# Kernel tuning notes

Hardware: AMD Instinct MI355X
Metric: run time of the kernel (lower is better)

The kernel has to match this reference:

```python
import jax, jax.numpy as jnp
import numpy as np

EPS_BIAS = 1e-6  # bias_epsilon

def _l2n(x, axis):
    # F.normalize: x / clamp_min(||x||, 1e-12)
    return x / jnp.maximum(jnp.linalg.norm(x, axis=axis, keepdims=True), 1e-12)

def _se3_W(w):
    # convex completion: rows sum to 1
    return jnp.concatenate([w, 1.0 - w.sum(-1, keepdims=True)], axis=-1)

def _vlin(v, W):
    # channel-mixing linear over dim 1 of [B, C, 3, N]
    return jnp.einsum('oc,bcdn->bodn', W, v)

def _vec_sub(v, w, b, se3):
    # sub VecLinear with s_in=s_out=0: linear + tiny normalized bias
    W = _se3_W(w) if se3 else w
    out = _vlin(v, W)
    bias = (_l2n(b, -1) * EPS_BIAS).reshape(1, -1, 1, 1)
    return out + bias

def _cev_norm(x):
    # channel_equi_vec_normalize
    d = _l2n(x, 2)
    n = jnp.linalg.norm(x, axis=2, keepdims=True)
    return d * _l2n(n, 1)

def setup_inputs() -> dict:
    key = jax.random.key(0)
    B, v_in, v_out, s_in, s_out, N = 8, 128, 128, 64, 64, 4096
    ks = jax.random.split(key, 16)
    def w(k, shape, fan):
        return jax.random.normal(k, shape, jnp.float32) / np.float32(np.sqrt(fan))
    return {
        'v_input': jax.random.normal(ks[0], (B, v_in, 3, N), jnp.float32),
        's_input': jax.random.normal(ks[1], (B, s_in, N), jnp.float32),
        'weight':   w(ks[2], (v_out, v_in - 1), v_in) + 1.0 / v_in,
        'sv_w':     w(ks[3], (v_out, s_in), s_in),
        'sv_b':     w(ks[4], (v_out,), s_in),
        'cross_w':  w(ks[5], (v_out, v_in - 1), v_in) + 1.0 / v_in,
        'cross_b':  jax.random.normal(ks[6], (v_out,), jnp.float32),
        'crossfc_w': w(ks[7], (v_out, 2 * v_out - 1), 2 * v_out) + 1.0 / (2 * v_out),
        'crossfc_b': jax.random.normal(ks[8], (v_out,), jnp.float32),
        'vsdir_w':  w(ks[9], (v_in, v_in), v_in),
        'vsdir_b':  jax.random.normal(ks[10], (v_in,), jnp.float32),
        'vs_w':     w(ks[11], (s_out, v_in), v_in),
        'vs_b':     w(ks[12], (s_out,), v_in),
        'ss_w':     w(ks[13], (s_out, s_in), s_in),
        'ss_b':     w(ks[14], (s_out,), s_in),
    }

def reference(v_input, s_input, weight, sv_w, sv_b, cross_w, cross_b,
              crossfc_w, crossfc_b, vsdir_w, vsdir_b, vs_w, vs_b, ss_w, ss_b):
    # --- vector linear (sim3/se3: convex weights) ---
    v_o = _vlin(v_input, _se3_W(weight))                      # [B, v_out, 3, N]
    # --- scalar -> vector invariant scale (normalized over channels) ---
    scale = jnp.einsum('os,bsn->bon', sv_w, s_input) + sv_b[None, :, None]
    scale = _l2n(scale, 1)                                    # [B, v_out, N]
    m = v_o.mean(axis=1, keepdims=True)
    v_o = (v_o - m) * scale[:, :, None, :] + m
    # --- cross-product branch ---
    v_dual = _vec_sub(v_input, cross_w, cross_b, True)
    dual_o = v_dual.mean(axis=1, keepdims=True)
    out_o = v_o.mean(axis=1, keepdims=True)
    v_cross = jnp.cross(_cev_norm(v_dual - dual_o), v_o - out_o, axis=2) + v_o
    v_o = _vec_sub(jnp.concatenate([v_cross, v_o], axis=1), crossfc_w, crossfc_b, True)
    # --- vector -> scalar (invariant) ---
    v_sR = v_input - v_input.mean(axis=1, keepdims=True)
    dual_dir = _l2n(_vec_sub(v_sR, vsdir_w, vsdir_b, False), 2)  # so3 sub-module
    s_from_v = _l2n((v_sR * dual_dir).sum(axis=2), 1)         # [B, v_in, N]
    s_from_v = jnp.einsum('oc,bcn->bon', vs_w, s_from_v) + vs_b[None, :, None]
    s_from_s = jnp.einsum('os,bsn->bon', ss_w, s_input) + ss_b[None, :, None]
    return v_o, s_from_s + s_from_v
```

## Files before the change

### kernel.cpp

```cpp
#include <hip/hip_runtime.h>

#define VOUT_ELEMS 12582912

typedef __attribute__((ext_vector_type(8))) short bf16x8;
typedef __attribute__((ext_vector_type(4))) float f32x4;

__device__ __forceinline__ unsigned short f2b(float f) {
  unsigned x = __float_as_uint(f);
  x = (x + 0x7FFFu + ((x >> 16) & 1u)) >> 16;
  return (unsigned short)x;
}
__device__ __forceinline__ float b2f(unsigned short u) {
  return __uint_as_float(((unsigned)u) << 16);
}
__device__ __forceinline__ unsigned pk2(float a, float b) {
  unsigned r;
  asm("v_cvt_pk_bf16_f32 %0, %1, %2" : "=v"(r) : "v"(a), "v"(b));
  return r;
}


__global__ void kprep0(const float* __restrict__ weight, const float* __restrict__ cross_w,
                       const float* __restrict__ crossfc_w, const float* __restrict__ vsdir_w,
                       const float* __restrict__ cross_b, const float* __restrict__ crossfc_b,
                       const float* __restrict__ vsdir_b, float* __restrict__ wsf)
{
  const int tid = threadIdx.x;
  const int l = tid & 63;
  const int wg = blockIdx.x*4 + (tid>>6);
#pragma unroll
  for (int k = 0; k < 2; ++k) {
    int o = wg*2 + k;
    float a = weight[o*127+l]  + ((l<63) ? weight[o*127+64+l]  : 0.f);
    float b = cross_w[o*127+l] + ((l<63) ? cross_w[o*127+64+l] : 0.f);
    float f = crossfc_w[o*255+l] + crossfc_w[o*255+64+l] + crossfc_w[o*255+128+l]
            + ((l<63) ? crossfc_w[o*255+192+l] : 0.f);
    float v = vsdir_w[o*128+l] + vsdir_w[o*128+64+l];
#pragma unroll
    for (int m = 1; m < 64; m <<= 1) {
      a += __shfl_xor(a,m,64); b += __shfl_xor(b,m,64);
      f += __shfl_xor(f,m,64); v += __shfl_xor(v,m,64);
    }
    if (l == 0) {
      wsf[384+o] = a; wsf[512+o] = b; wsf[640+o] = f; wsf[768+o] = v*(1.f/128.f);
    }
  }
  if (blockIdx.x == 0 && tid < 192) {
    const float* bsrc = (tid < 64) ? cross_b : (tid < 128 ? crossfc_b : vsdir_b);
    float a = 0.f;
    for (int i = l; i < 128; i += 64) { float t = bsrc[i]; a += t*t; }
#pragma unroll
    for (int m = 1; m < 64; m <<= 1) a += __shfl_xor(a,m,64);
    float nb = fmaxf(sqrtf(a), 1e-12f);
    for (int i = l; i < 128; i += 64)
      wsf[(tid>>6)*128 + i] = bsrc[i] / nb * 1e-6f;
  }
}

__global__ void kprep1(const float* __restrict__ weight, const float* __restrict__ sv_w,
                       const float* __restrict__ cross_w, const float* __restrict__ crossfc_w,
                       const float* __restrict__ vsdir_w, const float* __restrict__ vs_w,
                       const float* __restrict__ ss_w,
                       unsigned short* __restrict__ wsb, const float* __restrict__ wsf)
{
  const int stride = 64*256;
  const int base = blockIdx.x*256 + threadIdx.x;
  const float* rs1 = wsf+384; const float* rs2 = wsf+512;
  const float* rsF = wsf+640; const float* vdm = wsf+768;
  for (int i = base; i < 16384; i += stride) {
    int j=i&7, lane=(i>>3)&63, ks=(i>>9)&3, mt=i>>11;
    int o=16*mt+(lane&15), cc=32*ks+8*(lane>>4)+j;
    wsb[i]       = f2b(cc<127 ? weight[o*127+cc]  : 1.f-rs1[o]);
    wsb[16384+i] = f2b(cc<127 ? cross_w[o*127+cc] : 1.f-rs2[o]);
    wsb[65536+i] = f2b(vsdir_w[o*128+cc] - vdm[o]);
  }
  for (int i = base; i < 32768; i += stride) {
    int j=i&7, lane=(i>>3)&63, ks=(i>>9)&7, mt=i>>12;
    int o=16*mt+(lane&15), cc=32*ks+8*(lane>>4)+j;
    wsb[32768+i] = f2b(cc<255 ? crossfc_w[o*255+cc] : 1.f-rsF[o]);
  }
  for (int i = base; i < 8192; i += stride) {
    int j=i&7, lane=(i>>3)&63, ks=(i>>9)&1, mt=i>>10;
    int o=16*mt+(lane&15), s=32*ks+8*(lane>>4)+j;
    wsb[81920+i] = f2b(sv_w[o*64+s]);
  }
  for (int i = base; i < 8192; i += stride) {
    int j=i&7, lane=(i>>3)&63, ks=(i>>9)&3, mt=i>>11;
    int o=16*mt+(lane&15), c=32*ks+8*(lane>>4)+j;
    wsb[90112+i] = f2b(vs_w[o*128+c]);
  }
  for (int i = base; i < 4096; i += stride) {
    int j=i&7, lane=(i>>3)&63, ks=(i>>9)&1, mt=i>>10;
    int o=16*mt+(lane&15), s=32*ks+8*(lane>>4)+j;
    wsb[98304+i] = f2b(ss_w[o*64+s]);
  }
}

__global__ __launch_bounds__(256, 4) void kmain(
    const float* __restrict__ v_in, const float* __restrict__ s_in,
    const float* __restrict__ sv_b, const float* __restrict__ vs_b,
    const float* __restrict__ ss_b,
    const unsigned short* __restrict__ wsb, const float* __restrict__ wsf,
    float* __restrict__ out_v, float* __restrict__ out_s)
{
  __shared__ __align__(16) unsigned char smem[31744];
  unsigned short* bfr = (unsigned short*)smem;
  float* gmx          = (float*)(smem + 12288);
  float (*gred)[16][4]  = (float(*)[16][4])(smem + 12480);
  unsigned short* sfr = (unsigned short*)(smem + 24576);
  unsigned short* vfr = (unsigned short*)(smem + 26624);
  float (*gred2)[16][4] = (float(*)[16][4])(smem + 30720);

  const int tid = threadIdx.x;
  const int w = tid >> 6, l = tid & 63, h = l >> 4, c15 = l & 15;
  const int n0 = blockIdx.x * 16;
  const size_t bb = blockIdx.y;
  const size_t vbase = bb*384*4096 + n0;
  const size_t sbase = bb*64*4096 + n0;

  for (int i = tid; i < 384; i += 256) {
    int q = i & 3, d = (i >> 2) % 3, cq = i / 12;
    const float* src = &v_in[vbase + (size_t)(4*cq*3 + d)*4096 + 4*q];
    float4 x0 = *(const float4*)(src);
    float4 x1 = *(const float4*)(src + 3*4096);
    float4 x2 = *(const float4*)(src + 6*4096);
    float4 x3 = *(const float4*)(src + 9*4096);
    int slot = (cq >> 3)*3 + d;
    int hh = (cq >> 1) & 3;
    int jp = 2*(cq & 1);
    unsigned* bp = (unsigned*)bfr + (slot*64 + 16*hh + 4*q)*4 + jp;
    float a0[4]={x0.x,x0.y,x0.z,x0.w}, a1[4]={x1.x,x1.y,x1.z,x1.w};
    float a2[4]={x2.x,x2.y,x2.z,x2.w}, a3[4]={x3.x,x3.y,x3.z,x3.w};
#pragma unroll
    for (int e=0;e<4;++e)
      *(uint2*)(bp + e*4) = make_uint2(pk2(a0[e],a1[e]), pk2(a2[e],a3[e]));
  }
  if (tid < 64) {
    int q = tid & 3, sq = tid >> 2;
    const float* src = &s_in[sbase + (size_t)(4*sq)*4096 + 4*q];
    float4 x0 = *(const float4*)(src);
    float4 x1 = *(const float4*)(src + 4096);
    float4 x2 = *(const float4*)(src + 2*4096);
    float4 x3 = *(const float4*)(src + 3*4096);
    int slot = sq >> 3;
    int hh = (sq >> 1) & 3;
    int jp = 2*(sq & 1);
    unsigned* bp = (unsigned*)sfr + (slot*64 + 16*hh + 4*q)*4 + jp;
    float a0[4]={x0.x,x0.y,x0.z,x0.w}, a1[4]={x1.x,x1.y,x1.z,x1.w};
    float a2[4]={x2.x,x2.y,x2.z,x2.w}, a3[4]={x3.x,x3.y,x3.z,x3.w};
#pragma unroll
    for (int e=0;e<4;++e)
      *(uint2*)(bp + e*4) = make_uint2(pk2(a0[e],a1[e]), pk2(a2[e],a3[e]));
  }
  __syncthreads();

  const bf16x8* bv  = (const bf16x8*)bfr;
  const bf16x8* sfv_p = (const bf16x8*)sfr;
  const bf16x8* vfv_p = (const bf16x8*)vfr;
  const bf16x8* wv  = (const bf16x8*)wsb;
  const int obA = 16*w + 4*h, obB = 16*(w+4) + 4*h;

  f32x4 avo[2][3], adu[2][3], adr[2][3], asc[2];
  {
    f32x4 b2A = *(const f32x4*)&wsf[obA],     b2B = *(const f32x4*)&wsf[obB];
    f32x4 bdA = *(const f32x4*)&wsf[256+obA], bdB = *(const f32x4*)&wsf[256+obB];
#pragma unroll
    for (int d=0;d<3;++d) {
      avo[0][d]=(f32x4){0.f,0.f,0.f,0.f}; avo[1][d]=(f32x4){0.f,0.f,0.f,0.f};
      adu[0][d]=b2A; adu[1][d]=b2B;
      adr[0][d]=bdA; adr[1][d]=bdB;
    }
    asc[0] = *(const f32x4*)&sv_b[obA];
    asc[1] = *(const f32x4*)&sv_b[obB];
  }
#pragma unroll
  for (int ks=0;ks<4;++ks) {
    bf16x8 bx[3];
#pragma unroll
    for (int d=0;d<3;++d) bx[d] = bv[(ks*3+d)*64 + l];
#pragma unroll
    for (int mt=0;mt<2;++mt) {
      int fa = (w + 4*mt)*4 + ks;
      bf16x8 a1 = wv[fa*64 + l];
      bf16x8 a2 = wv[2048 + fa*64 + l];
      bf16x8 a3 = wv[8192 + fa*64 + l];
#pragma unroll
      for (int d=0;d<3;++d) {
        avo[mt][d] = __builtin_amdgcn_mfma_f32_16x16x32_bf16(a1, bx[d], avo[mt][d], 0,0,0);
        adu[mt][d] = __builtin_amdgcn_mfma_f32_16x16x32_bf16(a2, bx[d], adu[mt][d], 0,0,0);
        adr[mt][d] = __builtin_amdgcn_mfma_f32_16x16x32_bf16(a3, bx[d], adr[mt][d], 0,0,0);
      }
    }
  }
#pragma unroll
  for (int ks=0;ks<2;++ks) {
    bf16x8 bs = sfv_p[ks*64 + l];
#pragma unroll
    for (int mt=0;mt<2;++mt) {
      bf16x8 a4 = wv[10240 + ((w+4*mt)*2+ks)*64 + l];
      asc[mt] = __builtin_amdgcn_mfma_f32_16x16x32_bf16(a4, bs, asc[mt], 0,0,0);
    }
  }
  if (w < 3) {
    bf16x8 aone;
#pragma unroll
    for (int j=0;j<8;++j) aone[j] = (short)0x3C00;
    f32x4 amx = (f32x4){0.f,0.f,0.f,0.f};
#pragma unroll
    for (int ks=0;ks<4;++ks)
      amx = __builtin_amdgcn_mfma_f32_16x16x32_bf16(aone, bv[(ks*3+w)*64+l], amx, 0,0,0);
    if (h==0) gmx[16*w + c15] = amx[0];
  }

  {
    float red[8];
#pragma unroll
    for (int d=0;d<3;++d) {
      red[d]   = avo[0][d][0]+avo[0][d][1]+avo[0][d][2]+avo[0][d][3]
               + avo[1][d][0]+avo[1][d][1]+avo[1][d][2]+avo[1][d][3];
      red[3+d] = adu[0][d][0]+adu[0][d][1]+adu[0][d][2]+adu[0][d][3]
               + adu[1][d][0]+adu[1][d][1]+adu[1][d][2]+adu[1][d][3];
    }
    float q2 = 0.f;
#pragma unroll
    for (int mt=0;mt<2;++mt)
#pragma unroll
      for (int d=0;d<3;++d)
#pragma unroll
        for (int r=0;r<4;++r) q2 += adu[mt][d][r]*adu[mt][d][r];
    red[6] = q2;
    red[7] = asc[0][0]*asc[0][0]+asc[0][1]*asc[0][1]+asc[0][2]*asc[0][2]+asc[0][3]*asc[0][3]
           + asc[1][0]*asc[1][0]+asc[1][1]*asc[1][1]+asc[1][2]*asc[1][2]+asc[1][3]*asc[1][3];
#pragma unroll
    for (int m=16;m<64;m<<=1)
#pragma unroll
      for (int i=0;i<8;++i) red[i] += __shfl_xor(red[i], m, 64);
    if (h==0)
#pragma unroll
      for (int i=0;i<8;++i) gred[i][c15][w] = red[i];
  }
  __syncthreads();

  float mvo[3], mdu[3], mxv[3], d2s, sinv;
#pragma unroll
  for (int d=0;d<3;++d) {
    f32x4 t = *(const f32x4*)gred[d][c15];
    f32x4 u = *(const f32x4*)gred[3+d][c15];
    mvo[d] = (t[0]+t[1]+t[2]+t[3]) * (1.f/128.f);
    mdu[d] = (u[0]+u[1]+u[2]+u[3]) * (1.f/128.f);
    mxv[d] = gmx[16*d + c15];
  }
  { f32x4 t = *(const f32x4*)gred[6][c15]; d2s = t[0]+t[1]+t[2]+t[3]; }
  { f32x4 t = *(const f32x4*)gred[7][c15];
    sinv = 1.f / fmaxf(sqrtf(t[0]+t[1]+t[2]+t[3]), 1e-12f); }

  float po[3] = {0.f,0.f,0.f};
#pragma unroll
  for (int mt=0;mt<2;++mt)
#pragma unroll
    for (int r=0;r<4;++r) {
      float sk = asc[mt][r] * sinv;
#pragma unroll
      for (int d=0;d<3;++d) {
        float t = (avo[mt][d][r]-mvo[d])*sk + mvo[d];
        avo[mt][d][r] = t;
        po[d] += t;
      }
    }

  float sfvv[2][4]; float pfn = 0.f;
#pragma unroll
  for (int mt=0;mt<2;++mt) {
    int c0 = 16*(w+4*mt) + 4*h;
    int ks = c0 >> 5, hh = (c0>>3)&3, ju = 2*(h&1);
    float xr[3][4];
#pragma unroll
    for (int d=0;d<3;++d) {
      uint2 u = *(const uint2*)((const unsigned*)bfr + ((ks*3+d)*64 + 16*hh + c15)*4 + ju);
      xr[d][0]=b2f((unsigned short)u.x);  xr[d][1]=b2f((unsigned short)(u.x>>16));
      xr[d][2]=b2f((unsigned short)u.y);  xr[d][3]=b2f((unsigned short)(u.y>>16));
    }
#pragma unroll
    for (int r=0;r<4;++r) {
      float dx=adr[mt][0][r], dy=adr[mt][1][r], dz=adr[mt][2][r];
      float rn = sqrtf(dx*dx+dy*dy+dz*dz);
      float inv = 1.f/fmaxf(rn,1e-12f);
      float vx = xr[0][r]-mxv[0], vy = xr[1][r]-mxv[1], vz = xr[2][r]-mxv[2];
      float dot = (vx*dx+vy*dy+vz*dz)*inv;
      sfvv[mt][r] = dot; pfn += dot*dot;
    }
  }

  {
    float red2[4] = {po[0], po[1], po[2], pfn};
#pragma unroll
    for (int m=16;m<64;m<<=1)
#pragma unroll
      for (int i=0;i<4;++i) red2[i] += __shfl_xor(red2[i], m, 64);
    if (h==0)
#pragma unroll
      for (int i=0;i<4;++i) gred2[i][c15][w] = red2[i];
  }
  __syncthreads();

  float moo[3], sfni;
#pragma unroll
  for (int d=0;d<3;++d) {
    f32x4 t = *(const f32x4*)gred2[d][c15];
    moo[d] = (t[0]+t[1]+t[2]+t[3]) * (1.f/128.f);
  }
  { f32x4 t = *(const f32x4*)gred2[3][c15];
    sfni = 1.f/fmaxf(sqrtf(t[0]+t[1]+t[2]+t[3]), 1e-12f); }

  float m2 = mdu[0]*mdu[0]+mdu[1]*mdu[1]+mdu[2]*mdu[2];
  float F  = sqrtf(fmaxf(d2s - 128.f*m2, 0.f));
  float Fi = 1.f/fmaxf(F, 1e-12f);
#pragma unroll
  for (int mt=0;mt<2;++mt) {
    int c0 = 16*(w+4*mt) + 4*h;
    int ks = c0 >> 5, hh = (c0>>3)&3, ju = 2*(h&1);
    *(uint2*)((unsigned*)vfr + (ks*64 + 16*hh + c15)*4 + ju) =
      make_uint2(pk2(sfvv[mt][0]*sfni, sfvv[mt][1]*sfni),
                 pk2(sfvv[mt][2]*sfni, sfvv[mt][3]*sfni));
    float cv[3][4];
#pragma unroll
    for (int r=0;r<4;++r) {
      float ax=adu[mt][0][r]-mdu[0], ay=adu[mt][1][r]-mdu[1], az=adu[mt][2][r]-mdu[2];
      float rn = sqrtf(ax*ax+ay*ay+az*az);
      float s1 = (rn*Fi)/fmaxf(rn,1e-12f);
      ax*=s1; ay*=s1; az*=s1;
      float bx=avo[mt][0][r]-moo[0], by=avo[mt][1][r]-moo[1], bz=avo[mt][2][r]-moo[2];
      cv[0][r]=ay*bz-az*by+avo[mt][0][r];
      cv[1][r]=az*bx-ax*bz+avo[mt][1][r];
      cv[2][r]=ax*by-ay*bx+avo[mt][2][r];
    }
#pragma unroll
    for (int d=0;d<3;++d) {
      *(uint2*)((unsigned*)bfr + ((ks*3+d)*64 + 16*hh + c15)*4 + ju) =
        make_uint2(pk2(cv[d][0],cv[d][1]), pk2(cv[d][2],cv[d][3]));
      *(uint2*)((unsigned*)bfr + (((4+ks)*3+d)*64 + 16*hh + c15)*4 + ju) =
        make_uint2(pk2(avo[mt][d][0],avo[mt][d][1]), pk2(avo[mt][d][2],avo[mt][d][3]));
    }
  }
  __syncthreads();

  f32x4 afc[2][3];
  {
    f32x4 bfA = *(const f32x4*)&wsf[128+obA], bfB = *(const f32x4*)&wsf[128+obB];
#pragma unroll
    for (int d=0;d<3;++d) { afc[0][d]=bfA; afc[1][d]=bfB; }
  }
#pragma unroll
  for (int ks=0;ks<8;++ks) {
    bf16x8 bx[3];
#pragma unroll
    for (int d=0;d<3;++d) bx[d] = bv[(ks*3+d)*64 + l];
#pragma unroll
    for (int mt=0;mt<2;++mt) {
      bf16x8 a5 = wv[4096 + ((w+4*mt)*8+ks)*64 + l];
#pragma unroll
      for (int d=0;d<3;++d)
        afc[mt][d] = __builtin_amdgcn_mfma_f32_16x16x32_bf16(a5, bx[d], afc[mt][d], 0,0,0);
    }
  }
  f32x4 as2;
  {
    f32x4 bv1 = *(const f32x4*)&vs_b[obA];
    f32x4 bv2 = *(const f32x4*)&ss_b[obA];
    as2 = (f32x4){bv1[0]+bv2[0], bv1[1]+bv2[1], bv1[2]+bv2[2], bv1[3]+bv2[3]};
  }
#pragma unroll
  for (int ks=0;ks<4;++ks) {
    bf16x8 a6 = wv[11264 + (w*4+ks)*64 + l];
    as2 = __builtin_amdgcn_mfma_f32_16x16x32_bf16(a6, vfv_p[ks*64+l], as2, 0,0,0);
  }
#pragma unroll
  for (int ks=0;ks<2;++ks) {
    bf16x8 a7 = wv[12288 + (w*2+ks)*64 + l];
    as2 = __builtin_amdgcn_mfma_f32_16x16x32_bf16(a7, sfv_p[ks*64+l], as2, 0,0,0);
  }

#pragma unroll
  for (int mt=0;mt<2;++mt) {
    int c0 = 16*(w+4*mt) + 4*h;
#pragma unroll
    for (int d=0;d<3;++d)
#pragma unroll
      for (int r=0;r<4;++r)
        out_v[vbase + (size_t)((c0+r)*3 + d)*4096 + c15] = afc[mt][d][r];
  }
#pragma unroll
  for (int r=0;r<4;++r)
    out_s[sbase + (size_t)(obA+r)*4096 + c15] = as2[r];
}

extern "C" void kernel_launch(void* const* d_in, const int* in_sizes, int n_in,
                              void* d_out, int out_size, void* d_ws, size_t ws_size,
                              hipStream_t stream) {
  (void)in_sizes; (void)n_in; (void)out_size; (void)ws_size;
  const float* v_in      = (const float*)d_in[0];
  const float* s_in      = (const float*)d_in[1];
  const float* weight    = (const float*)d_in[2];
  const float* sv_w      = (const float*)d_in[3];
  const float* sv_b      = (const float*)d_in[4];
  const float* cross_w   = (const float*)d_in[5];
  const float* cross_b   = (const float*)d_in[6];
  const float* crossfc_w = (const float*)d_in[7];
  const float* crossfc_b = (const float*)d_in[8];
  const float* vsdir_w   = (const float*)d_in[9];
  const float* vsdir_b   = (const float*)d_in[10];
  const float* vs_w      = (const float*)d_in[11];
  const float* vs_b      = (const float*)d_in[12];
  const float* ss_w      = (const float*)d_in[13];
  const float* ss_b      = (const float*)d_in[14];

  unsigned short* wsb = (unsigned short*)d_ws;
  float* wsf = (float*)((char*)d_ws + 204800);

  kprep0<<<16, 256, 0, stream>>>(weight, cross_w, crossfc_w, vsdir_w,
                                 cross_b, crossfc_b, vsdir_b, wsf);
  kprep1<<<64, 256, 0, stream>>>(weight, sv_w, cross_w, crossfc_w, vsdir_w,
                                 vs_w, ss_w, wsb, wsf);
  dim3 grid(4096/16, 8);
  kmain<<<grid, 256, 0, stream>>>(v_in, s_in, sv_b, vs_b, ss_b, wsb, wsf,
                                  (float*)d_out, (float*)d_out + VOUT_ELEMS);
}
```

Before: 64.31 us.

## Fold second block reduction into first via algebraic mean and deferred normalization

Removes the second __syncthreads and its reduction round. The mean of the scaled v_o is now computed algebraically from extra first-pass sums (sum of avo*asc and sum of asc). The input-channel mean is computed by reduction instead of the ones-MFMA. The s_from_v normalization is deferred past the vs GEMM, since it is linear, and applied as a per-column scale at output, using the pfn reduction written to shared memory before the existing FC barrier. This costs more shuffle reductions (15 values instead of 8), more shared memory, and a bf16 rounding difference because unnormalized values are packed.

```diff
diff --git a/kernel.cpp b/kernel.cpp
--- a/kernel.cpp
+++ b/kernel.cpp
@@ -103,13 +103,12 @@
     const unsigned short* __restrict__ wsb, const float* __restrict__ wsf,
     float* __restrict__ out_v, float* __restrict__ out_s)
 {
-  __shared__ __align__(16) unsigned char smem[31744];
+  __shared__ __align__(16) unsigned char smem[34816];
   unsigned short* bfr = (unsigned short*)smem;
-  float* gmx          = (float*)(smem + 12288);
-  float (*gred)[16][4]  = (float(*)[16][4])(smem + 12480);
   unsigned short* sfr = (unsigned short*)(smem + 24576);
   unsigned short* vfr = (unsigned short*)(smem + 26624);
-  float (*gred2)[16][4] = (float(*)[16][4])(smem + 30720);
+  float (*gred)[16][4]  = (float(*)[16][4])(smem + 30720);
+  float (*gred2)[4]     = (float(*)[4])(smem + 34560);
 
   const int tid = threadIdx.x;
   const int w = tid >> 6, l = tid & 63, h = l >> 4, c15 = l & 15;
@@ -201,25 +200,34 @@
       asc[mt] = __builtin_amdgcn_mfma_f32_16x16x32_bf16(a4, bs, asc[mt], 0,0,0);
     }
   }
-  if (w < 3) {
-    bf16x8 aone;
-#pragma unroll
-    for (int j=0;j<8;++j) aone[j] = (short)0x3C00;
-    f32x4 amx = (f32x4){0.f,0.f,0.f,0.f};
-#pragma unroll
-    for (int ks=0;ks<4;++ks)
-      amx = __builtin_amdgcn_mfma_f32_16x16x32_bf16(aone, bv[(ks*3+w)*64+l], amx, 0,0,0);
-    if (h==0) gmx[16*w + c15] = amx[0];
+
+  float xr[2][3][4];
+#pragma unroll
+  for (int mt=0;mt<2;++mt) {
+    int c0 = 16*(w+4*mt) + 4*h;
+    int ksq = c0 >> 5, hh = (c0>>3)&3, ju = 2*(h&1);
+#pragma unroll
+    for (int d=0;d<3;++d) {
+      uint2 u = *(const uint2*)((const unsigned*)bfr + ((ksq*3+d)*64 + 16*hh + c15)*4 + ju);
+      xr[mt][d][0]=b2f((unsigned short)u.x);  xr[mt][d][1]=b2f((unsigned short)(u.x>>16));
+      xr[mt][d][2]=b2f((unsigned short)u.y);  xr[mt][d][3]=b2f((unsigned short)(u.y>>16));
+    }
   }
 
   {
-    float red[8];
+    float red[15];
 #pragma unroll
     for (int d=0;d<3;++d) {
       red[d]   = avo[0][d][0]+avo[0][d][1]+avo[0][d][2]+avo[0][d][3]
                + avo[1][d][0]+avo[1][d][1]+avo[1][d][2]+avo[1][d][3];
       red[3+d] = adu[0][d][0]+adu[0][d][1]+adu[0][d][2]+adu[0][d][3]
                + adu[1][d][0]+adu[1][d][1]+adu[1][d][2]+adu[1][d][3];
+      red[8+d] = avo[0][d][0]*asc[0][0]+avo[0][d][1]*asc[0][1]
+               + avo[0][d][2]*asc[0][2]+avo[0][d][3]*asc[0][3]
+               + avo[1][d][0]*asc[1][0]+avo[1][d][1]*asc[1][1]
+               + avo[1][d][2]*asc[1][2]+avo[1][d][3]*asc[1][3];
+      red[12+d] = xr[0][d][0]+xr[0][d][1]+xr[0][d][2]+xr[0][d][3]
+                + xr[1][d][0]+xr[1][d][1]+xr[1][d][2]+xr[1][d][3];
     }
     float q2 = 0.f;
 #pragma unroll
@@ -231,86 +239,60 @@
     red[6] = q2;
     red[7] = asc[0][0]*asc[0][0]+asc[0][1]*asc[0][1]+asc[0][2]*asc[0][2]+asc[0][3]*asc[0][3]
            + asc[1][0]*asc[1][0]+asc[1][1]*asc[1][1]+asc[1][2]*asc[1][2]+asc[1][3]*asc[1][3];
+    red[11]= asc[0][0]+asc[0][1]+asc[0][2]+asc[0][3]
+           + asc[1][0]+asc[1][1]+asc[1][2]+asc[1][3];
 #pragma unroll
     for (int m=16;m<64;m<<=1)
 #pragma unroll
-      for (int i=0;i<8;++i) red[i] += __shfl_xor(red[i], m, 64);
+      for (int i=0;i<15;++i) red[i] += __shfl_xor(red[i], m, 64);
     if (h==0)
 #pragma unroll
-      for (int i=0;i<8;++i) gred[i][c15][w] = red[i];
+      for (int i=0;i<15;++i) gred[i][c15][w] = red[i];
   }
   __syncthreads();
 
-  float mvo[3], mdu[3], mxv[3], d2s, sinv;
+  float mvo[3], mdu[3], mxv[3], moo[3], d2s, sinv, Sa;
+  { f32x4 t = *(const f32x4*)gred[7][c15];
+    sinv = 1.f / fmaxf(sqrtf(t[0]+t[1]+t[2]+t[3]), 1e-12f); }
+  { f32x4 t = *(const f32x4*)gred[11][c15]; Sa = t[0]+t[1]+t[2]+t[3]; }
+  { f32x4 t = *(const f32x4*)gred[6][c15];  d2s = t[0]+t[1]+t[2]+t[3]; }
 #pragma unroll
   for (int d=0;d<3;++d) {
     f32x4 t = *(const f32x4*)gred[d][c15];
     f32x4 u = *(const f32x4*)gred[3+d][c15];
+    f32x4 v = *(const f32x4*)gred[8+d][c15];
+    f32x4 x = *(const f32x4*)gred[12+d][c15];
     mvo[d] = (t[0]+t[1]+t[2]+t[3]) * (1.f/128.f);
     mdu[d] = (u[0]+u[1]+u[2]+u[3]) * (1.f/128.f);
-    mxv[d] = gmx[16*d + c15];
-  }
-  { f32x4 t = *(const f32x4*)gred[6][c15]; d2s = t[0]+t[1]+t[2]+t[3]; }
-  { f32x4 t = *(const f32x4*)gred[7][c15];
-    sinv = 1.f / fmaxf(sqrtf(t[0]+t[1]+t[2]+t[3]), 1e-12f); }
-
-  float po[3] = {0.f,0.f,0.f};
+    float Svs = v[0]+v[1]+v[2]+v[3];
+    moo[d] = mvo[d] + sinv*(Svs - mvo[d]*Sa)*(1.f/128.f);
+    mxv[d] = (x[0]+x[1]+x[2]+x[3]) * (1.f/128.f);
+  }
+
 #pragma unroll
   for (int mt=0;mt<2;++mt)
 #pragma unroll
     for (int r=0;r<4;++r) {
       float sk = asc[mt][r] * sinv;
 #pragma unroll
-      for (int d=0;d<3;++d) {
-        float t = (avo[mt][d][r]-mvo[d])*sk + mvo[d];
-        avo[mt][d][r] = t;
-        po[d] += t;
-      }
+      for (int d=0;d<3;++d)
+        avo[mt][d][r] = (avo[mt][d][r]-mvo[d])*sk + mvo[d];
     }
 
   float sfvv[2][4]; float pfn = 0.f;
 #pragma unroll
-  for (int mt=0;mt<2;++mt) {
-    int c0 = 16*(w+4*mt) + 4*h;
-    int ks = c0 >> 5, hh = (c0>>3)&3, ju = 2*(h&1);
-    float xr[3][4];
-#pragma unroll
-    for (int d=0;d<3;++d) {
-      uint2 u = *(const uint2*)((const unsigned*)bfr + ((ks*3+d)*64 + 16*hh + c15)*4 + ju);
-      xr[d][0]=b2f((unsigned short)u.x);  xr[d][1]=b2f((unsigned short)(u.x>>16));
-      xr[d][2]=b2f((unsigned short)u.y);  xr[d][3]=b2f((unsigned short)(u.y>>16));
-    }
+  for (int mt=0;mt<2;++mt)
 #pragma unroll
     for (int r=0;r<4;++r) {
       float dx=adr[mt][0][r], dy=adr[mt][1][r], dz=adr[mt][2][r];
       float rn = sqrtf(dx*dx+dy*dy+dz*dz);
       float inv = 1.f/fmaxf(rn,1e-12f);
-      float vx = xr[0][r]-mxv[0], vy = xr[1][r]-mxv[1], vz = xr[2][r]-mxv[2];
+      float vx = xr[mt][0][r]-mxv[0], vy = xr[mt][1][r]-mxv[1], vz = xr[mt][2][r]-mxv[2];
       float dot = (vx*dx+vy*dy+vz*dz)*inv;
       sfvv[mt][r] = dot; pfn += dot*dot;
     }
-  }
-
-  {
-    float red2[4] = {po[0], po[1], po[2], pfn};
-#pragma unroll
-    for (int m=16;m<64;m<<=1)
-#pragma unroll
-      for (int i=0;i<4;++i) red2[i] += __shfl_xor(red2[i], m, 64);
-    if (h==0)
-#pragma unroll
-      for (int i=0;i<4;++i) gred2[i][c15][w] = red2[i];
-  }
-  __syncthreads();
-
-  float moo[3], sfni;
-#pragma unroll
-  for (int d=0;d<3;++d) {
-    f32x4 t = *(const f32x4*)gred2[d][c15];
-    moo[d] = (t[0]+t[1]+t[2]+t[3]) * (1.f/128.f);
-  }
-  { f32x4 t = *(const f32x4*)gred2[3][c15];
-    sfni = 1.f/fmaxf(sqrtf(t[0]+t[1]+t[2]+t[3]), 1e-12f); }
+  pfn += __shfl_xor(pfn,16,64); pfn += __shfl_xor(pfn,32,64);
+  if (h==0) gred2[c15][w] = pfn;
 
   float m2 = mdu[0]*mdu[0]+mdu[1]*mdu[1]+mdu[2]*mdu[2];
   float F  = sqrtf(fmaxf(d2s - 128.f*m2, 0.f));
@@ -318,10 +300,9 @@
 #pragma unroll
   for (int mt=0;mt<2;++mt) {
     int c0 = 16*(w+4*mt) + 4*h;
-    int ks = c0 >> 5, hh = (c0>>3)&3, ju = 2*(h&1);
-    *(uint2*)((unsigned*)vfr + (ks*64 + 16*hh + c15)*4 + ju) =
-      make_uint2(pk2(sfvv[mt][0]*sfni, sfvv[mt][1]*sfni),
-                 pk2(sfvv[mt][2]*sfni, sfvv[mt][3]*sfni));
+    int ksq = c0 >> 5, hh = (c0>>3)&3, ju = 2*(h&1);
+    *(uint2*)((unsigned*)vfr + (ksq*64 + 16*hh + c15)*4 + ju) =
+      make_uint2(pk2(sfvv[mt][0], sfvv[mt][1]), pk2(sfvv[mt][2], sfvv[mt][3]));
     float cv[3][4];
 #pragma unroll
     for (int r=0;r<4;++r) {
@@ -336,9 +317,9 @@
     }
 #pragma unroll
     for (int d=0;d<3;++d) {
-      *(uint2*)((unsigned*)bfr + ((ks*3+d)*64 + 16*hh + c15)*4 + ju) =
+      *(uint2*)((unsigned*)bfr + ((ksq*3+d)*64 + 16*hh + c15)*4 + ju) =
         make_uint2(pk2(cv[d][0],cv[d][1]), pk2(cv[d][2],cv[d][3]));
-      *(uint2*)((unsigned*)bfr + (((4+ks)*3+d)*64 + 16*hh + c15)*4 + ju) =
+      *(uint2*)((unsigned*)bfr + (((4+ksq)*3+d)*64 + 16*hh + c15)*4 + ju) =
         make_uint2(pk2(avo[mt][d][0],avo[mt][d][1]), pk2(avo[mt][d][2],avo[mt][d][3]));
     }
   }
@@ -363,22 +344,26 @@
         afc[mt][d] = __builtin_amdgcn_mfma_f32_16x16x32_bf16(a5, bx[d], afc[mt][d], 0,0,0);
     }
   }
-  f32x4 as2;
+  f32x4 as_v = (f32x4){0.f,0.f,0.f,0.f};
+#pragma unroll
+  for (int ks=0;ks<4;++ks) {
+    bf16x8 a6 = wv[11264 + (w*4+ks)*64 + l];
+    as_v = __builtin_amdgcn_mfma_f32_16x16x32_bf16(a6, vfv_p[ks*64+l], as_v, 0,0,0);
+  }
+  f32x4 as_s;
   {
     f32x4 bv1 = *(const f32x4*)&vs_b[obA];
     f32x4 bv2 = *(const f32x4*)&ss_b[obA];
-    as2 = (f32x4){bv1[0]+bv2[0], bv1[1]+bv2[1], bv1[2]+bv2[2], bv1[3]+bv2[3]};
-  }
-#pragma unroll
-  for (int ks=0;ks<4;++ks) {
-    bf16x8 a6 = wv[11264 + (w*4+ks)*64 + l];
-    as2 = __builtin_amdgcn_mfma_f32_16x16x32_bf16(a6, vfv_p[ks*64+l], as2, 0,0,0);
+    as_s = (f32x4){bv1[0]+bv2[0], bv1[1]+bv2[1], bv1[2]+bv2[2], bv1[3]+bv2[3]};
   }
 #pragma unroll
   for (int ks=0;ks<2;++ks) {
     bf16x8 a7 = wv[12288 + (w*2+ks)*64 + l];
-    as2 = __builtin_amdgcn_mfma_f32_16x16x32_bf16(a7, sfv_p[ks*64+l], as2, 0,0,0);
-  }
+    as_s = __builtin_amdgcn_mfma_f32_16x16x32_bf16(a7, sfv_p[ks*64+l], as_s, 0,0,0);
+  }
+  float sfni;
+  { f32x4 t = *(const f32x4*)gred2[c15];
+    sfni = 1.f/fmaxf(sqrtf(t[0]+t[1]+t[2]+t[3]), 1e-12f); }
 
 #pragma unroll
   for (int mt=0;mt<2;++mt) {
@@ -391,7 +376,7 @@
   }
 #pragma unroll
   for (int r=0;r<4;++r)
-    out_s[sbase + (size_t)(obA+r)*4096 + c15] = as2[r];
+    out_s[sbase + (size_t)(obA+r)*4096 + c15] = as_s[r] + as_v[r]*sfni;
 }
 
 extern "C" void kernel_launch(void* const* d_in, const int* in_sizes, int n_in,
```

Result: slower. 94.06 us (+46.3%).

## Split output-channel tiles across 8 waves instead of 2 tiles per wave

Applied to the files above, without the earlier changes.

Doubles the block to 512 threads so each wave owns one 16-channel M-tile rather than two. The cross-wave reductions widen to 8 partial slots, and the staging and scalar-output work are remapped to the new thread ranges. The aim is to cut per-wave accumulator registers and serial MFMA chains so more waves can hide latency. In exchange the B fragments are loaded from LDS by twice as many waves, and the larger block may limit residency per CU.

```diff
diff --git a/kernel.cpp b/kernel.cpp
--- a/kernel.cpp
+++ b/kernel.cpp
@@ -96,20 +96,21 @@
   }
 }
 
-__global__ __launch_bounds__(256, 4) void kmain(
+__global__ __launch_bounds__(512) __attribute__((amdgpu_waves_per_eu(4)))
+void kmain(
     const float* __restrict__ v_in, const float* __restrict__ s_in,
     const float* __restrict__ sv_b, const float* __restrict__ vs_b,
     const float* __restrict__ ss_b,
     const unsigned short* __restrict__ wsb, const float* __restrict__ wsf,
     float* __restrict__ out_v, float* __restrict__ out_s)
 {
-  __shared__ __align__(16) unsigned char smem[31744];
+  __shared__ __align__(16) unsigned char smem[32768];
   unsigned short* bfr = (unsigned short*)smem;
   float* gmx          = (float*)(smem + 12288);
-  float (*gred)[16][4]  = (float(*)[16][4])(smem + 12480);
+  float (*gred)[16][8]  = (float(*)[16][8])(smem + 12480);
   unsigned short* sfr = (unsigned short*)(smem + 24576);
   unsigned short* vfr = (unsigned short*)(smem + 26624);
-  float (*gred2)[16][4] = (float(*)[16][4])(smem + 30720);
+  float (*gred2)[16][8] = (float(*)[16][8])(smem + 30720);
 
   const int tid = threadIdx.x;
   const int w = tid >> 6, l = tid & 63, h = l >> 4, c15 = l & 15;
@@ -118,7 +119,8 @@
   const size_t vbase = bb*384*4096 + n0;
   const size_t sbase = bb*64*4096 + n0;
 
-  for (int i = tid; i < 384; i += 256) {
+  if (tid < 384) {
+    int i = tid;
     int q = i & 3, d = (i >> 2) % 3, cq = i / 12;
     const float* src = &v_in[vbase + (size_t)(4*cq*3 + d)*4096 + 4*q];
     float4 x0 = *(const float4*)(src);
@@ -134,9 +136,9 @@
 #pragma unroll
     for (int e=0;e<4;++e)
       *(uint2*)(bp + e*4) = make_uint2(pk2(a0[e],a1[e]), pk2(a2[e],a3[e]));
-  }
-  if (tid < 64) {
-    int q = tid & 3, sq = tid >> 2;
+  } else if (tid < 448) {
+    int st = tid - 384;
+    int q = st & 3, sq = st >> 2;
     const float* src = &s_in[sbase + (size_t)(4*sq)*4096 + 4*q];
     float4 x0 = *(const float4*)(src);
     float4 x1 = *(const float4*)(src + 4096);
@@ -158,48 +160,40 @@
   const bf16x8* sfv_p = (const bf16x8*)sfr;
   const bf16x8* vfv_p = (const bf16x8*)vfr;
   const bf16x8* wv  = (const bf16x8*)wsb;
-  const int obA = 16*w + 4*h, obB = 16*(w+4) + 4*h;
-
-  f32x4 avo[2][3], adu[2][3], adr[2][3], asc[2];
-  {
-    f32x4 b2A = *(const f32x4*)&wsf[obA],     b2B = *(const f32x4*)&wsf[obB];
-    f32x4 bdA = *(const f32x4*)&wsf[256+obA], bdB = *(const f32x4*)&wsf[256+obB];
-#pragma unroll
-    for (int d=0;d<3;++d) {
-      avo[0][d]=(f32x4){0.f,0.f,0.f,0.f}; avo[1][d]=(f32x4){0.f,0.f,0.f,0.f};
-      adu[0][d]=b2A; adu[1][d]=b2B;
-      adr[0][d]=bdA; adr[1][d]=bdB;
-    }
-    asc[0] = *(const f32x4*)&sv_b[obA];
-    asc[1] = *(const f32x4*)&sv_b[obB];
+  const int obA = 16*w + 4*h;
+
+  f32x4 avo[3], adu[3], adr[3], asc;
+  {
+    f32x4 b2A = *(const f32x4*)&wsf[obA];
+    f32x4 bdA = *(const f32x4*)&wsf[256+obA];
+#pragma unroll
+    for (int d=0;d<3;++d) {
+      avo[d]=(f32x4){0.f,0.f,0.f,0.f};
+      adu[d]=b2A;
+      adr[d]=bdA;
+    }
+    asc = *(const f32x4*)&sv_b[obA];
   }
 #pragma unroll
   for (int ks=0;ks<4;++ks) {
     bf16x8 bx[3];
 #pragma unroll
     for (int d=0;d<3;++d) bx[d] = bv[(ks*3+d)*64 + l];
-#pragma unroll
-    for (int mt=0;mt<2;++mt) {
-      int fa = (w + 4*mt)*4 + ks;
-      bf16x8 a1 = wv[fa*64 + l];
-      bf16x8 a2 = wv[2048 + fa*64 + l];
-      bf16x8 a3 = wv[8192 + fa*64 + l];
-#pragma unroll
-      for (int d=0;d<3;++d) {
-        avo[mt][d] = __builtin_amdgcn_mfma_f32_16x16x32_bf16(a1, bx[d], avo[mt][d], 0,0,0);
-        adu[mt][d] = __builtin_amdgcn_mfma_f32_16x16x32_bf16(a2, bx[d], adu[mt][d], 0,0,0);
-        adr[mt][d] = __builtin_amdgcn_mfma_f32_16x16x32_bf16(a3, bx[d], adr[mt][d], 0,0,0);
-      }
+    int fa = w*4 + ks;
+    bf16x8 a1 = wv[fa*64 + l];
+    bf16x8 a2 = wv[2048 + fa*64 + l];
+    bf16x8 a3 = wv[8192 + fa*64 + l];
+#pragma unroll
+    for (int d=0;d<3;++d) {
+      avo[d] = __builtin_amdgcn_mfma_f32_16x16x32_bf16(a1, bx[d], avo[d], 0,0,0);
+      adu[d] = __builtin_amdgcn_mfma_f32_16x16x32_bf16(a2, bx[d], adu[d], 0,0,0);
+      adr[d] = __builtin_amdgcn_mfma_f32_16x16x32_bf16(a3, bx[d], adr[d], 0,0,0);
     }
   }
 #pragma unroll
   for (int ks=0;ks<2;++ks) {
-    bf16x8 bs = sfv_p[ks*64 + l];
-#pragma unroll
-    for (int mt=0;mt<2;++mt) {
-      bf16x8 a4 = wv[10240 + ((w+4*mt)*2+ks)*64 + l];
-      asc[mt] = __builtin_amdgcn_mfma_f32_16x16x32_bf16(a4, bs, asc[mt], 0,0,0);
-    }
+    bf16x8 a4 = wv[10240 + (w*2+ks)*64 + l];
+    asc = __builtin_amdgcn_mfma_f32_16x16x32_bf16(a4, sfv_p[ks*64+l], asc, 0,0,0);
   }
   if (w < 3) {
     bf16x8 aone;
@@ -216,21 +210,16 @@
     float red[8];
 #pragma unroll
     for (int d=0;d<3;++d) {
-      red[d]   = avo[0][d][0]+avo[0][d][1]+avo[0][d][2]+avo[0][d][3]
-               + avo[1][d][0]+avo[1][d][1]+avo[1][d][2]+avo[1][d][3];
-      red[3+d] = adu[0][d][0]+adu[0][d][1]+adu[0][d][2]+adu[0][d][3]
-               + adu[1][d][0]+adu[1][d][1]+adu[1][d][2]+adu[1][d][3];
+      red[d]   = avo[d][0]+avo[d][1]+avo[d][2]+avo[d][3];
+      red[3+d] = adu[d][0]+adu[d][1]+adu[d][2]+adu[d][3];
     }
     float q2 = 0.f;
 #pragma unroll
-    for (int mt=0;mt<2;++mt)
-#pragma unroll
-      for (int d=0;d<3;++d)
-#pragma unroll
-        for (int r=0;r<4;++r) q2 += adu[mt][d][r]*adu[mt][d][r];
+    for (int d=0;d<3;++d)
+#pragma unroll
+      for (int r=0;r<4;++r) q2 += adu[d][r]*adu[d][r];
     red[6] = q2;
-    red[7] = asc[0][0]*asc[0][0]+asc[0][1]*asc[0][1]+asc[0][2]*asc[0][2]+asc[0][3]*asc[0][3]
-           + asc[1][0]*asc[1][0]+asc[1][1]*asc[1][1]+asc[1][2]*asc[1][2]+asc[1][3]*asc[1][3];
+    red[7] = asc[0]*asc[0]+asc[1]*asc[1]+asc[2]*asc[2]+asc[3]*asc[3];
 #pragma unroll
     for (int m=16;m<64;m<<=1)
 #pragma unroll
@@ -244,50 +233,52 @@
   float mvo[3], mdu[3], mxv[3], d2s, sinv;
 #pragma unroll
   for (int d=0;d<3;++d) {
-    f32x4 t = *(const f32x4*)gred[d][c15];
-    f32x4 u = *(const f32x4*)gred[3+d][c15];
-    mvo[d] = (t[0]+t[1]+t[2]+t[3]) * (1.f/128.f);
-    mdu[d] = (u[0]+u[1]+u[2]+u[3]) * (1.f/128.f);
+    const f32x4* p  = (const f32x4*)gred[d][c15];
+    const f32x4* p2 = (const f32x4*)gred[3+d][c15];
+    f32x4 t0=p[0], t1=p[1], u0=p2[0], u1=p2[1];
+    mvo[d] = (t0[0]+t0[1]+t0[2]+t0[3]+t1[0]+t1[1]+t1[2]+t1[3]) * (1.f/128.f);
+    mdu[d] = (u0[0]+u0[1]+u0[2]+u0[3]+u1[0]+u1[1]+u1[2]+u1[3]) * (1.f/128.f);
     mxv[d] = gmx[16*d + c15];
   }
-  { f32x4 t = *(const f32x4*)gred[6][c15]; d2s = t[0]+t[1]+t[2]+t[3]; }
-  { f32x4 t = *(const f32x4*)gred[7][c15];
-    sinv = 1.f / fmaxf(sqrtf(t[0]+t[1]+t[2]+t[3]), 1e-12f); }
+  { const f32x4* p = (const f32x4*)gred[6][c15];
+    f32x4 t0=p[0], t1=p[1];
+    d2s = t0[0]+t0[1]+t0[2]+t0[3]+t1[0]+t1[1]+t1[2]+t1[3]; }
+  { const f32x4* p = (const f32x4*)gred[7][c15];
+    f32x4 t0=p[0], t1=p[1];
+    sinv = 1.f / fmaxf(sqrtf(t0[0]+t0[1]+t0[2]+t0[3]+t1[0]+t1[1]+t1[2]+t1[3]), 1e-12f); }
 
   float po[3] = {0.f,0.f,0.f};
 #pragma unroll
-  for (int mt=0;mt<2;++mt)
-#pragma unroll
-    for (int r=0;r<4;++r) {
-      float sk = asc[mt][r] * sinv;
-#pragma unroll
-      for (int d=0;d<3;++d) {
-        float t = (avo[mt][d][r]-mvo[d])*sk + mvo[d];
-        avo[mt][d][r] = t;
-        po[d] += t;
-      }
-    }
-
-  float sfvv[2][4]; float pfn = 0.f;
-#pragma unroll
-  for (int mt=0;mt<2;++mt) {
-    int c0 = 16*(w+4*mt) + 4*h;
-    int ks = c0 >> 5, hh = (c0>>3)&3, ju = 2*(h&1);
+  for (int r=0;r<4;++r) {
+    float sk = asc[r] * sinv;
+#pragma unroll
+    for (int d=0;d<3;++d) {
+      float t = (avo[d][r]-mvo[d])*sk + mvo[d];
+      avo[d][r] = t;
+      po[d] += t;
+    }
+  }
+
+  const int ksq = w >> 1;
+  const int hh2 = 2*(w&1) + (h>>1);
+  const int ju = 2*(h&1);
+  float sfvv[4]; float pfn = 0.f;
+  {
     float xr[3][4];
 #pragma unroll
     for (int d=0;d<3;++d) {
-      uint2 u = *(const uint2*)((const unsigned*)bfr + ((ks*3+d)*64 + 16*hh + c15)*4 + ju);
+      uint2 u = *(const uint2*)((const unsigned*)bfr + ((ksq*3+d)*64 + 16*hh2 + c15)*4 + ju);
       xr[d][0]=b2f((unsigned short)u.x);  xr[d][1]=b2f((unsigned short)(u.x>>16));
       xr[d][2]=b2f((unsigned short)u.y);  xr[d][3]=b2f((unsigned short)(u.y>>16));
     }
 #pragma unroll
     for (int r=0;r<4;++r) {
-      float dx=adr[mt][0][r], dy=adr[mt][1][r], dz=adr[mt][2][r];
+      float dx=adr[0][r], dy=adr[1][r], dz=adr[2][r];
       float rn = sqrtf(dx*dx+dy*dy+dz*dz);
       float inv = 1.f/fmaxf(rn,1e-12f);
       float vx = xr[0][r]-mxv[0], vy = xr[1][r]-mxv[1], vz = xr[2][r]-mxv[2];
       float dot = (vx*dx+vy*dy+vz*dz)*inv;
-      sfvv[mt][r] = dot; pfn += dot*dot;
+      sfvv[r] = dot; pfn += dot*dot;
     }
   }
 
@@ -306,92 +297,86 @@
   float moo[3], sfni;
 #pragma unroll
   for (int d=0;d<3;++d) {
-    f32x4 t = *(const f32x4*)gred2[d][c15];
-    moo[d] = (t[0]+t[1]+t[2]+t[3]) * (1.f/128.f);
-  }
-  { f32x4 t = *(const f32x4*)gred2[3][c15];
-    sfni = 1.f/fmaxf(sqrtf(t[0]+t[1]+t[2]+t[3]), 1e-12f); }
+    const f32x4* p = (const f32x4*)gred2[d][c15];
+    f32x4 t0=p[0], t1=p[1];
+    moo[d] = (t0[0]+t0[1]+t0[2]+t0[3]+t1[0]+t1[1]+t1[2]+t1[3]) * (1.f/128.f);
+  }
+  { const f32x4* p = (const f32x4*)gred2[3][c15];
+    f32x4 t0=p[0], t1=p[1];
+    sfni = 1.f/fmaxf(sqrtf(t0[0]+t0[1]+t0[2]+t0[3]+t1[0]+t1[1]+t1[2]+t1[3]), 1e-12f); }
 
   float m2 = mdu[0]*mdu[0]+mdu[1]*mdu[1]+mdu[2]*mdu[2];
   float F  = sqrtf(fmaxf(d2s - 128.f*m2, 0.f));
   float Fi = 1.f/fmaxf(F, 1e-12f);
-#pragma unroll
-  for (int mt=0;mt<2;++mt) {
-    int c0 = 16*(w+4*mt) + 4*h;
-    int ks = c0 >> 5, hh = (c0>>3)&3, ju = 2*(h&1);
-    *(uint2*)((unsigned*)vfr + (ks*64 + 16*hh + c15)*4 + ju) =
-      make_uint2(pk2(sfvv[mt][0]*sfni, sfvv[mt][1]*sfni),
-                 pk2(sfvv[mt][2]*sfni, sfvv[mt][3]*sfni));
+  {
+    *(uint2*)((unsigned*)vfr + (ksq*64 + 16*hh2 + c15)*4 + ju) =
+      make_uint2(pk2(sfvv[0]*sfni, sfvv[1]*sfni),
+                 pk2(sfvv[2]*sfni, sfvv[3]*sfni));
     float cv[3][4];
 #pragma unroll
     for (int r=0;r<4;++r) {
-      float ax=adu[mt][0][r]-mdu[0], ay=adu[mt][1][r]-mdu[1], az=adu[mt][2][r]-mdu[2];
+      float ax=adu[0][r]-mdu[0], ay=adu[1][r]-mdu[1], az=adu[2][r]-mdu[2];
       float rn = sqrtf(ax*ax+ay*ay+az*az);
       float s1 = (rn*Fi)/fmaxf(rn,1e-12f);
       ax*=s1; ay*=s1; az*=s1;
-      float bx=avo[mt][0][r]-moo[0], by=avo[mt][1][r]-moo[1], bz=avo[mt][2][r]-moo[2];
-      cv[0][r]=ay*bz-az*by+avo[mt][0][r];
-      cv[1][r]=az*bx-ax*bz+avo[mt][1][r];
-      cv[2][r]=ax*by-ay*bx+avo[mt][2][r];
-    }
-#pragma unroll
-    for (int d=0;d<3;++d) {
-      *(uint2*)((unsigned*)bfr + ((ks*3+d)*64 + 16*hh + c15)*4 + ju) =
+      float bx=avo[0][r]-moo[0], by=avo[1][r]-moo[1], bz=avo[2][r]-moo[2];
+      cv[0][r]=ay*bz-az*by+avo[0][r];
+      cv[1][r]=az*bx-ax*bz+avo[1][r];
+      cv[2][r]=ax*by-ay*bx+avo[2][r];
+    }
+#pragma unroll
+    for (int d=0;d<3;++d) {
+      *(uint2*)((unsigned*)bfr + ((ksq*3+d)*64 + 16*hh2 + c15)*4 + ju) =
         make_uint2(pk2(cv[d][0],cv[d][1]), pk2(cv[d][2],cv[d][3]));
-      *(uint2*)((unsigned*)bfr + (((4+ks)*3+d)*64 + 16*hh + c15)*4 + ju) =
-        make_uint2(pk2(avo[mt][d][0],avo[mt][d][1]), pk2(avo[mt][d][2],avo[mt][d][3]));
+      *(uint2*)((unsigned*)bfr + (((4+ksq)*3+d)*64 + 16*hh2 + c15)*4 + ju) =
+        make_uint2(pk2(avo[d][0],avo[d][1]), pk2(avo[d][2],avo[d][3]));
     }
   }
   __syncthreads();
 
-  f32x4 afc[2][3];
-  {
-    f32x4 bfA = *(const f32x4*)&wsf[128+obA], bfB = *(const f32x4*)&wsf[128+obB];
-#pragma unroll
-    for (int d=0;d<3;++d) { afc[0][d]=bfA; afc[1][d]=bfB; }
+  f32x4 afc[3];
+  {
+    f32x4 bfA = *(const f32x4*)&wsf[128+obA];
+#pragma unroll
+    for (int d=0;d<3;++d) afc[d]=bfA;
   }
 #pragma unroll
   for (int ks=0;ks<8;++ks) {
     bf16x8 bx[3];
 #pragma unroll
     for (int d=0;d<3;++d) bx[d] = bv[(ks*3+d)*64 + l];
-#pragma unroll
-    for (int mt=0;mt<2;++mt) {
-      bf16x8 a5 = wv[4096 + ((w+4*mt)*8+ks)*64 + l];
-#pragma unroll
-      for (int d=0;d<3;++d)
-        afc[mt][d] = __builtin_amdgcn_mfma_f32_16x16x32_bf16(a5, bx[d], afc[mt][d], 0,0,0);
-    }
-  }
-  f32x4 as2;
-  {
-    f32x4 bv1 = *(const f32x4*)&vs_b[obA];
-    f32x4 bv2 = *(const f32x4*)&ss_b[obA];
-    as2 = (f32x4){bv1[0]+bv2[0], bv1[1]+bv2[1], bv1[2]+bv2[2], bv1[3]+bv2[3]};
-  }
-#pragma unroll
-  for (int ks=0;ks<4;++ks) {
-    bf16x8 a6 = wv[11264 + (w*4+ks)*64 + l];
-    as2 = __builtin_amdgcn_mfma_f32_16x16x32_bf16(a6, vfv_p[ks*64+l], as2, 0,0,0);
-  }
-#pragma unroll
-  for (int ks=0;ks<2;++ks) {
-    bf16x8 a7 = wv[12288 + (w*2+ks)*64 + l];
-    as2 = __builtin_amdgcn_mfma_f32_16x16x32_bf16(a7, sfv_p[ks*64+l], as2, 0,0,0);
-  }
-
-#pragma unroll
-  for (int mt=0;mt<2;++mt) {
-    int c0 = 16*(w+4*mt) + 4*h;
+    bf16x8 a5 = wv[4096 + (w*8+ks)*64 + l];
 #pragma unroll
     for (int d=0;d<3;++d)
-#pragma unroll
-      for (int r=0;r<4;++r)
-        out_v[vbase + (size_t)((c0+r)*3 + d)*4096 + c15] = afc[mt][d][r];
-  }
-#pragma unroll
-  for (int r=0;r<4;++r)
-    out_s[sbase + (size_t)(obA+r)*4096 + c15] = as2[r];
+      afc[d] = __builtin_amdgcn_mfma_f32_16x16x32_bf16(a5, bx[d], afc[d], 0,0,0);
+  }
+  if (w < 4) {
+    f32x4 as2;
+    {
+      f32x4 bv1 = *(const f32x4*)&vs_b[obA];
+      f32x4 bv2 = *(const f32x4*)&ss_b[obA];
+      as2 = (f32x4){bv1[0]+bv2[0], bv1[1]+bv2[1], bv1[2]+bv2[2], bv1[3]+bv2[3]};
+    }
+#pragma unroll
+    for (int ks=0;ks<4;++ks) {
+      bf16x8 a6 = wv[11264 + (w*4+ks)*64 + l];
+      as2 = __builtin_amdgcn_mfma_f32_16x16x32_bf16(a6, vfv_p[ks*64+l], as2, 0,0,0);
+    }
+#pragma unroll
+    for (int ks=0;ks<2;++ks) {
+      bf16x8 a7 = wv[12288 + (w*2+ks)*64 + l];
+      as2 = __builtin_amdgcn_mfma_f32_16x16x32_bf16(a7, sfv_p[ks*64+l], as2, 0,0,0);
+    }
+#pragma unroll
+    for (int r=0;r<4;++r)
+      out_s[sbase + (size_t)(obA+r)*4096 + c15] = as2[r];
+  }
+
+#pragma unroll
+  for (int d=0;d<3;++d)
+#pragma unroll
+    for (int r=0;r<4;++r)
+      out_v[vbase + (size_t)((obA+r)*3 + d)*4096 + c15] = afc[d][r];
 }
 
 extern "C" void kernel_launch(void* const* d_in, const int* in_sizes, int n_in,
@@ -422,6 +407,6 @@
   kprep1<<<64, 256, 0, stream>>>(weight, sv_w, cross_w, crossfc_w, vsdir_w,
                                  vs_w, ss_w, wsb, wsf);
   dim3 grid(4096/16, 8);
-  kmain<<<grid, 256, 0, stream>>>(v_in, s_in, sv_b, vs_b, ss_b, wsb, wsf,
+  kmain<<<grid, 512, 0, stream>>>(v_in, s_in, sv_b, vs_b, ss_b, wsb, wsf,
                                   (float*)d_out, (float*)d_out + VOUT_ELEMS);
 }
```

After: 64.21 us. Within noise of the previous version (-0.2%).
